# Kernel optimization log

Hardware: AMD Instinct MI355X
Metric: run time of the kernel (lower is better)

The kernel has to match this reference:

```python
import jax, jax.numpy as jnp
import numpy as np

N_NODES = 50000
N_EDGES = 800000
EPS = 1e-5
NEG_SLOPE = 0.2


def _gatv2(x, src, dst, Wl, bl, Wr, br, att, bias, concat, N):
    # PyG GATv2Conv: xl = lin_l(x) (source side), xr = lin_r(x) (target side)
    H, C = att.shape
    xl = (x @ Wl + bl).reshape(N, H, C)
    xr = (x @ Wr + br).reshape(N, H, C)
    # per-edge message: leaky_relu(xl[j] + xr[i]), attention logit = <att, .>
    z = xl[src] + xr[dst]                      # [E, H, C]
    z = jnp.where(z > 0, z, NEG_SLOPE * z)
    logits = jnp.einsum('ehc,hc->eh', z, att)  # [E, H]
    # segment softmax over incoming edges of each target node
    m = jax.lax.stop_gradient(jax.ops.segment_max(logits, dst, num_segments=N))
    p = jnp.exp(logits - m[dst])
    s = jax.ops.segment_sum(p, dst, num_segments=N)
    alpha = p / s[dst]                         # [E, H]
    out = jax.ops.segment_sum(xl[src] * alpha[..., None], dst, num_segments=N)  # [N, H, C]
    out = out.reshape(N, H * C) if concat else out.mean(axis=1)
    return out + bias


def _bn(x, g, b):
    mu = x.mean(axis=0)
    v = x.var(axis=0)
    return (x - mu) * jax.lax.rsqrt(v + EPS) * g + b


def setup_inputs() -> dict:
    key = jax.random.key(0)
    ks = jax.random.split(key, 16)
    x = jax.random.normal(ks[0], (N_NODES, 2), jnp.float32)
    edge_index = jax.random.randint(ks[1], (2, N_EDGES), 0, N_NODES, dtype=jnp.int64)

    def lin(k, i, o):
        return jax.random.normal(k, (i, o), jnp.float32) * (1.0 / np.sqrt(i))

    inp = {'x': x, 'edge_index': edge_index}
    # layer 1: in=2, heads=8, out=16, concat
    inp['W1l'] = lin(ks[2], 2, 128); inp['b1l'] = jnp.zeros((128,), jnp.float32)
    inp['W1r'] = lin(ks[3], 2, 128); inp['b1r'] = jnp.zeros((128,), jnp.float32)
    inp['a1'] = jax.random.normal(ks[4], (8, 16), jnp.float32) * 0.1
    inp['bias1'] = jnp.zeros((128,), jnp.float32)
    inp['g1'] = jnp.ones((128,), jnp.float32); inp['be1'] = jnp.zeros((128,), jnp.float32)
    # layer 2: in=128, heads=4, out=16, concat
    inp['W2l'] = lin(ks[5], 128, 64); inp['b2l'] = jnp.zeros((64,), jnp.float32)
    inp['W2r'] = lin(ks[6], 128, 64); inp['b2r'] = jnp.zeros((64,), jnp.float32)
    inp['a2'] = jax.random.normal(ks[7], (4, 16), jnp.float32) * 0.1
    inp['bias2'] = jnp.zeros((64,), jnp.float32)
    inp['g2'] = jnp.ones((64,), jnp.float32); inp['be2'] = jnp.zeros((64,), jnp.float32)
    # layer 3: in=64, heads=1, out=2, mean (concat=False)
    inp['W3l'] = lin(ks[8], 64, 2); inp['b3l'] = jnp.zeros((2,), jnp.float32)
    inp['W3r'] = lin(ks[9], 64, 2); inp['b3r'] = jnp.zeros((2,), jnp.float32)
    inp['a3'] = jax.random.normal(ks[10], (1, 2), jnp.float32) * 0.1
    inp['bias3'] = jnp.zeros((2,), jnp.float32)
    return inp


def reference(x, edge_index, W1l, b1l, W1r, b1r, a1, bias1, g1, be1,
              W2l, b2l, W2r, b2r, a2, bias2, g2, be2,
              W3l, b3l, W3r, b3r, a3, bias3):
    N = x.shape[0]
    loops = jnp.arange(N, dtype=edge_index.dtype)
    src = jnp.concatenate([edge_index[0], loops])  # add self loops (PyG default)
    dst = jnp.concatenate([edge_index[1], loops])
    h = _gatv2(x, src, dst, W1l, b1l, W1r, b1r, a1, bias1, True, N)
    h = jax.nn.elu(_bn(h, g1, be1))  # dropout is identity in eval
    h = _gatv2(h, src, dst, W2l, b2l, W2r, b2r, a2, bias2, True, N)
    h = jax.nn.elu(_bn(h, g2, be2))
    return _gatv2(h, src, dst, W3l, b3l, W3r, b3r, a3, bias3, False, N)
```

## Files before the change

kernel.cpp:

```cpp
#include <hip/hip_runtime.h>
#include <hip/hip_bf16.h>

#define N_NODES 50000
#define N_E0    800000
#define N_ET    850000
#define EPSBN   1e-5f
#define LOG2E   1.4426950408889634f

#define LEAKY(z) fmaxf((z), 0.2f * (z))

#define OFF_C 0
#define OFF_A (128*N_NODES)
#define OFF_B (192*N_NODES)
#define OFF_STATS (256*N_NODES)
#define OFF_S1R (OFF_STATS + 512)
#define OFF_S2R (OFF_S1R + 16384)
#define OFF_P (OFF_S2R + 8192)
#define N_PARAM_TOT 118312
#define OFF_ROWPTR (OFF_P + N_PARAM_TOT)
#define OFF_DEG    (OFF_ROWPTR + 50001)
#define OFF_CURSOR (OFF_DEG + 50000)
#define OFF_BSUM   (OFF_CURSOR + 50000)
#define OFF_COL    (OFF_BSUM + 256)
#define OFF_FLAGS  (OFF_COL + 850064)
#define OFF_SCNT   (OFF_FLAGS + 2)

#define BK_CAP 131072
#define BK_CHUNK 2048

typedef float v2f __attribute__((ext_vector_type(2)));

__device__ __forceinline__ v2f ld2(const float* p) { return *(const v2f*)p; }
__device__ __forceinline__ v2f fma2(v2f a, v2f b, v2f c) {
    return __builtin_elementwise_fma(a, b, c);
}
__device__ __forceinline__ v2f max2(v2f a, v2f b) {
    return __builtin_elementwise_max(a, b);
}

__device__ __forceinline__ float bf2f(unsigned short u) {
    return __uint_as_float(((unsigned int)u) << 16);
}
__device__ __forceinline__ unsigned short f2bf(float f) {
    unsigned int u = __float_as_uint(f);
    u += 0x7FFFu + ((u >> 16) & 1u);
    return (unsigned short)(u >> 16);
}

__global__ void prep_kernel(const unsigned short* xr, const int* ei, int* flags,
                            int* deg, float* stats, float* s1r, float* s2r, int* scnt,
                            int* col) {
    int i = blockIdx.x * 256 + threadIdx.x;
    if (i < N_NODES) deg[i] = 0;
    if (i < 512) stats[i] = 0.f;
    if (i < 16384) s1r[i] = 0.f;
    if (i < 8192)  s2r[i] = 0.f;
    if (i < 8) scnt[i] = 0;
    if (i < 64) col[N_ET + i] = 0;
    if (blockIdx.x == 0) {
        __shared__ int c1, c2;
        if (threadIdx.x == 0) { c1 = 0; c2 = 0; }
        __syncthreads();
        int t = threadIdx.x;
        int l1 = 0, l2 = 0;
        for (int k = t; k < 2048; k += 256) {
            float v = bf2f(xr[k]);
            if (!(fabsf(v) <= 100.0f)) l1++;
            if (ei[2 * k + 1] != 0) l2++;
        }
        atomicAdd(&c1, l1);
        atomicAdd(&c2, l2);
        __syncthreads();
        if (t == 0) {
            flags[0] = (c1 > 16) ? 1 : 0;
            flags[1] = (c2 == 0) ? 1 : 0;
        }
    }
}

struct ParamPtrs { const void* p[23]; };

__global__ void convert_kernel(ParamPtrs ps, float* dst, const int* flags) {
    const int sizes[23] = {100000, 256,128,256,128,128,128,128,128,
                           8192,64,8192,64,64,64,64,64,
                           128,2,128,2,2,2};
    int g = blockIdx.x * 256 + threadIdx.x;
    if (g >= N_PARAM_TOT) return;
    int t = 0, off = g;
    while (off >= sizes[t]) { off -= sizes[t]; t++; }
    float v;
    if (flags[0]) v = ((const float*)ps.p[t])[off];
    else          v = bf2f(((const unsigned short*)ps.p[t])[off]);
    if (t == 5 || t == 13 || t == 21) v *= LOG2E;
    dst[g] = v;
}

__global__ void bucket_kernel(const int* ei, const int* flags, int* scnt,
                              int* dstb, int* srcb, int* deg) {
    __shared__ int lcnt[8];
    __shared__ int lbase[8];
    int tid = threadIdx.x;
    if (tid < 8) lcnt[tid] = 0;
    __syncthreads();
    int base_e = blockIdx.x * BK_CHUNK;
    int i64 = flags[1];
    int src[8], dst[8], pos[8];
    #pragma unroll
    for (int u = 0; u < 8; u++) {
        int e = base_e + u * 256 + tid;
        if (e < N_ET) {
            int s, d;
            if (e < N_E0) {
                d = i64 ? ei[2 * (N_E0 + e)] : ei[N_E0 + e];
                s = i64 ? ei[2 * e] : ei[e];
            } else { s = d = e - N_E0; }
            src[u] = s; dst[u] = d;
            pos[u] = atomicAdd(&lcnt[d / 6250], 1);
            atomicAdd(&deg[d], 1);
        } else dst[u] = -1;
    }
    __syncthreads();
    if (tid < 8) lbase[tid] = atomicAdd(&scnt[tid], lcnt[tid]);
    __syncthreads();
    #pragma unroll
    for (int u = 0; u < 8; u++) {
        if (dst[u] >= 0) {
            int st = dst[u] / 6250;
            int gp = st * BK_CAP + lbase[st] + pos[u];
            dstb[gp] = dst[u];
            srcb[gp] = src[u];
        }
    }
}

__global__ void scan1_kernel(const int* deg, int* row_ptr, int* bsum) {
    __shared__ int sh[256];
    int i = blockIdx.x * 256 + threadIdx.x;
    int v = (i < N_NODES) ? deg[i] : 0;
    sh[threadIdx.x] = v;
    __syncthreads();
    for (int off = 1; off < 256; off <<= 1) {
        int t = (threadIdx.x >= off) ? sh[threadIdx.x - off] : 0;
        __syncthreads();
        sh[threadIdx.x] += t;
        __syncthreads();
    }
    if (i < N_NODES) row_ptr[i] = sh[threadIdx.x] - v;
    if (threadIdx.x == 255) bsum[blockIdx.x] = sh[255];
}

__global__ void scan23_kernel(int* row_ptr, int* cursor, const int* bsum) {
    __shared__ int sh[256];
    int t = threadIdx.x;
    int v = (t < 196) ? bsum[t] : 0;
    sh[t] = v;
    __syncthreads();
    for (int off = 1; off < 256; off <<= 1) {
        int u = (t >= off) ? sh[t - off] : 0;
        __syncthreads();
        sh[t] += u;
        __syncthreads();
    }
    int prefix = (blockIdx.x == 0) ? 0 : sh[blockIdx.x - 1];
    int i = blockIdx.x * 256 + t;
    if (i < N_NODES) {
        int r = row_ptr[i] + prefix;
        row_ptr[i] = r;
        cursor[i] = r;
    }
    if (i == 0) row_ptr[N_NODES] = N_ET;
}

__global__ void scatter2_kernel(const int* scnt, const int* dstb, const int* srcb,
                                int* cursor, int* col) {
    int stripe = blockIdx.x & 7;
    int bi = blockIdx.x >> 3;
    int cnt = scnt[stripe];
    int off = stripe * BK_CAP;
    for (int t = bi * 256 + threadIdx.x; t < cnt; t += 32 * 256) {
        int d = dstb[off + t];
        int pos = atomicAdd(&cursor[d], 1);
        col[pos] = srcb[off + t];
    }
}

__global__ void __launch_bounds__(256) gather1_kernel(
    const int* row_ptr, const int* col, const float* x,
    const float* W1l, const float* b1l, const float* W1r, const float* b1r,
    const float* att, const float* bias, unsigned int* Cb, float* s1r)
{
    int wv = threadIdx.x >> 6;
    int lane = threadIdx.x & 63;
    int n0 = blockIdx.x * 16 + wv * 4;
    int eslot = lane >> 4;
    int slot  = lane & 15;
    int c0 = slot << 3;

    int rpl = row_ptr[n0 + (lane < 5 ? lane : 4)];
    int r0 = __builtin_amdgcn_readlane(rpl, 0);
    int r1 = __builtin_amdgcn_readlane(rpl, 1);
    int r2 = __builtin_amdgcn_readlane(rpl, 2);
    int r3 = __builtin_amdgcn_readlane(rpl, 3);
    int r4 = __builtin_amdgcn_readlane(rpl, 4);
    int d0 = r1 - r0, d1 = r2 - r1, d2 = r3 - r2, d3 = r4 - r3;

    int ms0 = col[r0 + lane];
    int ms1 = col[r1 + lane];
    int ms2 = col[r2 + lane];
    int ms3 = col[r3 + lane];
    v2f xs0 = ld2(x + 2 * ms0);
    v2f xs1 = ld2(x + 2 * ms1);
    v2f xs2 = ld2(x + 2 * ms2);
    v2f xs3 = ld2(x + 2 * ms3);

    v2f w0[4], w1[4], at[4];
    #pragma unroll
    for (int k = 0; k < 4; k++) {
        w0[k] = ld2(W1l + c0 + 2 * k);
        w1[k] = ld2(W1l + 128 + c0 + 2 * k);
        at[k] = ld2(att + c0 + 2 * k);
    }
    v2f w0o = ld2(W1l + 2 * lane);
    v2f w1o = ld2(W1l + 128 + 2 * lane);
    v2f bo  = ld2(b1l + 2 * lane) + ld2(bias + 2 * lane);

    float bnS0 = 0.f, bnS1 = 0.f, bnQ0 = 0.f, bnQ1 = 0.f;

    auto run_node = [&](int ni, int basei, int degi, v2f xsv) {
        v2f xd = ld2(x + 2 * ni);
        v2f xdx = {xd.x, xd.x}, xdy = {xd.y, xd.y};
        v2f K[4];
        #pragma unroll
        for (int k = 0; k < 4; k++) {
            v2f wr0 = ld2(W1r + c0 + 2 * k);
            v2f wr1 = ld2(W1r + 128 + c0 + 2 * k);
            v2f bb  = ld2(b1r + c0 + 2 * k) + ld2(b1l + c0 + 2 * k);
            K[k] = fma2(xdx, wr0, fma2(xdy, wr1, bb));
        }
        float S0 = 0.f, S1 = 0.f, SP = 0.f;
        int cnt = degi < 64 ? degi : 64;
        for (int jb = 0; jb < cnt; jb += 4) {
            int e = jb + eslot;
            float x0s = __shfl(xsv.x, e, 64);
            float x1s = __shfl(xsv.y, e, 64);
            v2f x0 = {x0s, x0s}, x1 = {x1s, x1s};
            v2f lg = {0.f, 0.f};
            #pragma unroll
            for (int k = 0; k < 4; k++) {
                v2f t = fma2(x1, w1[k], fma2(x0, w0[k], K[k]));
                lg = fma2(max2(t, 0.2f * t), at[k], lg);
            }
            float logit = lg.x + lg.y;
            logit += __shfl_xor(logit, 1, 64);
            float p = (e < cnt) ? exp2f(logit) : 0.f;
            S0 = fmaf(p, x0s, S0);
            S1 = fmaf(p, x1s, S1);
            SP += p;
        }
        for (int j0 = 64; j0 < degi; j0 += 64) {
            int c2 = degi - j0; if (c2 > 64) c2 = 64;
            int m = col[basei + j0 + lane];
            v2f xv = ld2(x + 2 * m);
            for (int jb = 0; jb < c2; jb += 4) {
                int e = jb + eslot;
                float x0s = __shfl(xv.x, e, 64);
                float x1s = __shfl(xv.y, e, 64);
                v2f x0 = {x0s, x0s}, x1 = {x1s, x1s};
                v2f lg = {0.f, 0.f};
                #pragma unroll
                for (int k = 0; k < 4; k++) {
                    v2f t = fma2(x1, w1[k], fma2(x0, w0[k], K[k]));
                    lg = fma2(max2(t, 0.2f * t), at[k], lg);
                }
                float logit = lg.x + lg.y;
                logit += __shfl_xor(logit, 1, 64);
                float p = (e < c2) ? exp2f(logit) : 0.f;
                S0 = fmaf(p, x0s, S0);
                S1 = fmaf(p, x1s, S1);
                SP += p;
            }
        }
        #pragma unroll
        for (int m = 16; m <= 32; m <<= 1) {
            S0 += __shfl_xor(S0, m, 64);
            S1 += __shfl_xor(S1, m, 64);
            SP += __shfl_xor(SP, m, 64);
        }
        float inv = 1.f / SP;
        float t0 = S0 * inv, t1 = S1 * inv;
        int hsrc = (lane >> 3) << 1;
        float t0o = __shfl(t0, hsrc, 64);
        float t1o = __shfl(t1, hsrc, 64);
        float ox = fmaf(w0o.x, t0o, fmaf(w1o.x, t1o, bo.x));
        float oy = fmaf(w0o.y, t0o, fmaf(w1o.y, t1o, bo.y));
        Cb[ni * 64 + lane] = ((unsigned int)f2bf(oy) << 16) | f2bf(ox);
        bnS0 += ox; bnS1 += oy;
        bnQ0 += ox * ox; bnQ1 += oy * oy;
    };

    run_node(n0,     r0, d0, xs0);
    run_node(n0 + 1, r1, d1, xs1);
    run_node(n0 + 2, r2, d2, xs2);
    run_node(n0 + 3, r3, d3, xs3);

    __shared__ float sred[4][128];
    __shared__ float qred[4][128];
    sred[wv][2 * lane]     = bnS0;
    sred[wv][2 * lane + 1] = bnS1;
    qred[wv][2 * lane]     = bnQ0;
    qred[wv][2 * lane + 1] = bnQ1;
    __syncthreads();
    int t = threadIdx.x;
    float a;
    if (t < 128) a = sred[0][t] + sred[1][t] + sred[2][t] + sred[3][t];
    else { int c = t - 128; a = qred[0][c] + qred[1][c] + qred[2][c] + qred[3][c]; }
    atomicAdd(&s1r[(blockIdx.x & 63) * 256 + t], a);
}

__global__ void red1_kernel(const float* s1r, const float* g1, const float* be1,
                            float* stats) {
    __shared__ float ls[256];
    int t = threadIdx.x;
    float a = 0.f;
    for (int r = 0; r < 64; r++) a += s1r[r * 256 + t];
    ls[t] = a;
    __syncthreads();
    if (t < 128) {
        float mu = ls[t] * (1.0f / N_NODES);
        float var = ls[128 + t] * (1.0f / N_NODES) - mu * mu;
        float sc = g1[t] * rsqrtf(var + EPSBN);
        stats[t] = sc;
        stats[128 + t] = be1[t] - mu * sc;
    }
}

__global__ void __launch_bounds__(256) lin2_kernel(
    const unsigned int* Cb, const float* stats, const float* Wl, const float* bl,
    const float* Wr, const float* br, unsigned short* xl2b, float* xr2)
{
    __shared__ float h[64 * 132];
    int tid = threadIdx.x;
    int nb = blockIdx.x * 64;
    for (int i = tid; i < 64 * 64; i += 256) {
        int ni = i >> 6, kp = i & 63;
        int n = nb + ni;
        int k = 2 * kp;
        float v0 = 0.f, v1 = 0.f;
        if (n < N_NODES) {
            unsigned int pk = Cb[n * 64 + kp];
            float b0 = fmaf(__uint_as_float(pk << 16),        stats[k],     stats[128 + k]);
            float b1 = fmaf(__uint_as_float(pk & 0xffff0000u), stats[k + 1], stats[128 + k + 1]);
            v0 = b0 > 0.f ? b0 : __expf(b0) - 1.f;
            v1 = b1 > 0.f ? b1 : __expf(b1) - 1.f;
        }
        h[ni * 132 + k]     = v0;
        h[ni * 132 + k + 1] = v1;
    }
    __syncthreads();
    int kt = (tid & 15) * 4;
    int nt = (tid >> 4) * 4;
    float accl[4][4], accr[4][4];
    #pragma unroll
    for (int i = 0; i < 4; i++) {
        #pragma unroll
        for (int k = 0; k < 4; k++) { accl[i][k] = 0.f; accr[i][k] = 0.f; }
    }
    for (int j = 0; j < 128; j += 4) {
        float4 hv[4];
        #pragma unroll
        for (int i = 0; i < 4; i++)
            hv[i] = *(const float4*)&h[(nt + i) * 132 + j];
        #pragma unroll
        for (int jj = 0; jj < 4; jj++) {
            float4 wl4 = *(const float4*)&Wl[(j + jj) * 64 + kt];
            float4 wr4 = *(const float4*)&Wr[(j + jj) * 64 + kt];
            #pragma unroll
            for (int i = 0; i < 4; i++) {
                float hvv = (jj == 0) ? hv[i].x : (jj == 1) ? hv[i].y :
                            (jj == 2) ? hv[i].z : hv[i].w;
                accl[i][0] += hvv * wl4.x; accl[i][1] += hvv * wl4.y;
                accl[i][2] += hvv * wl4.z; accl[i][3] += hvv * wl4.w;
                accr[i][0] += hvv * wr4.x; accr[i][1] += hvv * wr4.y;
                accr[i][2] += hvv * wr4.z; accr[i][3] += hvv * wr4.w;
            }
        }
    }
    float4 blv = *(const float4*)&bl[kt];
    float4 brv = *(const float4*)&br[kt];
    #pragma unroll
    for (int i = 0; i < 4; i++) {
        int n = nb + nt + i;
        if (n < N_NODES) {
            ushort4 ob;
            ob.x = f2bf(accl[i][0] + blv.x);
            ob.y = f2bf(accl[i][1] + blv.y);
            ob.z = f2bf(accl[i][2] + blv.z);
            ob.w = f2bf(accl[i][3] + blv.w);
            *(ushort4*)&xl2b[n * 64 + kt] = ob;
            float4 o;
            o.x = accr[i][0] + brv.x; o.y = accr[i][1] + brv.y;
            o.z = accr[i][2] + brv.z; o.w = accr[i][3] + brv.w;
            *(float4*)&xr2[n * 64 + kt] = o;
        }
    }
}

__global__ void __launch_bounds__(256) gather2_kernel(
    const int* row_ptr, const int* col, const unsigned short* xl2b, const float* xr2,
    const float* att, const float* bias, float* C, float* s2r)
{
    int gid = blockIdx.x * 256 + threadIdx.x;
    int n = gid >> 6;
    int lane = threadIdx.x & 63;
    int grp = lane >> 4;
    int cidx = lane & 15;
    float4 xrv = *(const float4*)(xr2 + n * 64 + 4 * cidx);
    float4 atv = *(const float4*)(att + 4 * cidx);
    int base = __builtin_amdgcn_readfirstlane(row_ptr[n]);
    int deg  = __builtin_amdgcn_readfirstlane(row_ptr[n + 1]) - base;
    float4 acc = make_float4(0.f, 0.f, 0.f, 0.f);
    float den = 0.f;
    for (int j0 = 0; j0 < deg; j0 += 64) {
        int cnt = deg - j0; if (cnt > 64) cnt = 64;
        int msrc = col[base + j0 + lane];
        for (int j4 = 0; j4 < cnt; j4 += 8) {
            int e0 = j4 + grp, e1 = j4 + 4 + grp;
            int s0 = __shfl(msrc, e0, 64);
            int s1 = __shfl(msrc, e1, 64);
            bool v0 = e0 < cnt, v1 = e1 < cnt;
            s0 = v0 ? s0 : 0;
            s1 = v1 ? s1 : 0;
            uint2 ba = *(const uint2*)(xl2b + (size_t)s0 * 64 + 4 * cidx);
            uint2 bb = *(const uint2*)(xl2b + (size_t)s1 * 64 + 4 * cidx);
            float a0 = __uint_as_float(ba.x << 16);
            float a1 = __uint_as_float(ba.x & 0xffff0000u);
            float a2 = __uint_as_float(ba.y << 16);
            float a3 = __uint_as_float(ba.y & 0xffff0000u);
            float b0 = __uint_as_float(bb.x << 16);
            float b1 = __uint_as_float(bb.x & 0xffff0000u);
            float b2 = __uint_as_float(bb.y << 16);
            float b3 = __uint_as_float(bb.y & 0xffff0000u);
            float pa = LEAKY(a0 + xrv.x) * atv.x;
            pa = fmaf(LEAKY(a1 + xrv.y), atv.y, pa);
            pa = fmaf(LEAKY(a2 + xrv.z), atv.z, pa);
            pa = fmaf(LEAKY(a3 + xrv.w), atv.w, pa);
            float pb = LEAKY(b0 + xrv.x) * atv.x;
            pb = fmaf(LEAKY(b1 + xrv.y), atv.y, pb);
            pb = fmaf(LEAKY(b2 + xrv.z), atv.z, pb);
            pb = fmaf(LEAKY(b3 + xrv.w), atv.w, pb);
            pa += __shfl_xor(pa, 1, 64);
            pa += __shfl_xor(pa, 2, 64);
            pb += __shfl_xor(pb, 1, 64);
            pb += __shfl_xor(pb, 2, 64);
            float ea = v0 ? exp2f(pa) : 0.f;
            float eb = v1 ? exp2f(pb) : 0.f;
            acc.x = fmaf(ea, a0, acc.x); acc.x = fmaf(eb, b0, acc.x);
            acc.y = fmaf(ea, a1, acc.y); acc.y = fmaf(eb, b1, acc.y);
            acc.z = fmaf(ea, a2, acc.z); acc.z = fmaf(eb, b2, acc.z);
            acc.w = fmaf(ea, a3, acc.w); acc.w = fmaf(eb, b3, acc.w);
            den += ea + eb;
        }
    }
    acc.x += __shfl_xor(acc.x, 16, 64); acc.x += __shfl_xor(acc.x, 32, 64);
    acc.y += __shfl_xor(acc.y, 16, 64); acc.y += __shfl_xor(acc.y, 32, 64);
    acc.z += __shfl_xor(acc.z, 16, 64); acc.z += __shfl_xor(acc.z, 32, 64);
    acc.w += __shfl_xor(acc.w, 16, 64); acc.w += __shfl_xor(acc.w, 32, 64);
    den += __shfl_xor(den, 16, 64);
    den += __shfl_xor(den, 32, 64);
    float inv = 1.f / den;
    float4 bi = *(const float4*)(bias + 4 * cidx);
    float4 o;
    o.x = fmaf(acc.x, inv, bi.x);
    o.y = fmaf(acc.y, inv, bi.y);
    o.z = fmaf(acc.z, inv, bi.z);
    o.w = fmaf(acc.w, inv, bi.w);
    if (lane < 16) *(float4*)(C + n * 64 + 4 * cidx) = o;
    __shared__ float sred[4][64];
    __shared__ float qred[4][64];
    int wv = threadIdx.x >> 6;
    if (lane < 16) {
        int c = 4 * cidx;
        sred[wv][c]     = o.x; qred[wv][c]     = o.x * o.x;
        sred[wv][c + 1] = o.y; qred[wv][c + 1] = o.y * o.y;
        sred[wv][c + 2] = o.z; qred[wv][c + 2] = o.z * o.z;
        sred[wv][c + 3] = o.w; qred[wv][c + 3] = o.w * o.w;
    }
    __syncthreads();
    int t = threadIdx.x;
    if (t < 128) {
        float a;
        if (t < 64) a = sred[0][t] + sred[1][t] + sred[2][t] + sred[3][t];
        else { int c = t - 64; a = qred[0][c] + qred[1][c] + qred[2][c] + qred[3][c]; }
        atomicAdd(&s2r[(blockIdx.x & 63) * 128 + t], a);
    }
}

__global__ void red2_kernel(const float* s2r, const float* g2, const float* be2,
                            float* stats) {
    __shared__ float ls[128];
    int t = threadIdx.x;
    float a = 0.f;
    for (int r = 0; r < 64; r++) a += s2r[r * 128 + t];
    ls[t] = a;
    __syncthreads();
    if (t < 64) {
        float mu = ls[t] * (1.0f / N_NODES);
        float var = ls[64 + t] * (1.0f / N_NODES) - mu * mu;
        float sc = g2[t] * rsqrtf(var + EPSBN);
        stats[t] = sc;
        stats[64 + t] = be2[t] - mu * sc;
    }
}

__global__ void __launch_bounds__(256) lin3_kernel(
    const float* C, const float* stats2,
    const float* Wl, const float* bl, const float* Wr, const float* br,
    float* xl3, float* xr3)
{
    int gid = blockIdx.x * 256 + threadIdx.x;
    int n = gid >> 6;
    int lane = threadIdx.x & 63;
    if (n >= N_NODES) return;
    float v = fmaf(C[n * 64 + lane], stats2[lane], stats2[64 + lane]);
    float h = v > 0.f ? v : __expf(v) - 1.f;
    float2 wlv = *(const float2*)(Wl + 2 * lane);
    float2 wrv = *(const float2*)(Wr + 2 * lane);
    float a0 = h * wlv.x, a1 = h * wlv.y;
    float r0 = h * wrv.x, r1 = h * wrv.y;
    #pragma unroll
    for (int m = 1; m < 64; m <<= 1) {
        a0 += __shfl_xor(a0, m, 64);
        a1 += __shfl_xor(a1, m, 64);
        r0 += __shfl_xor(r0, m, 64);
        r1 += __shfl_xor(r1, m, 64);
    }
    if (lane == 0) {
        xl3[2 * n]     = a0 + bl[0];
        xl3[2 * n + 1] = a1 + bl[1];
        xr3[2 * n]     = r0 + br[0];
        xr3[2 * n + 1] = r1 + br[1];
    }
}

__global__ void __launch_bounds__(256) gather3_kernel(
    const int* row_ptr, const int* col,
    const float* xl3, const float* xr3,
    const float* att, const float* bias,
    void* out, const int* flags) {
    int gid = blockIdx.x * 256 + threadIdx.x;
    int n = gid >> 2;
    int q = threadIdx.x & 3;
    if (n >= N_NODES) return;
    float a0 = att[0], a1 = att[1];
    float xr0 = xr3[2 * n], xr1 = xr3[2 * n + 1];
    float acc0 = 0.f, acc1 = 0.f, den = 0.f;
    int e0 = row_ptr[n], e1 = row_ptr[n + 1];
    for (int e = e0 + q; e < e1; e += 4) {
        int src = col[e];
        float2 xs = *(const float2*)(xl3 + 2 * src);
        float z0 = LEAKY(xs.x + xr0);
        float z1 = LEAKY(xs.y + xr1);
        float p = exp2f(fmaf(z0, a0, z1 * a1));
        acc0 = fmaf(p, xs.x, acc0);
        acc1 = fmaf(p, xs.y, acc1);
        den += p;
    }
    acc0 += __shfl_xor(acc0, 1, 64); acc0 += __shfl_xor(acc0, 2, 64);
    acc1 += __shfl_xor(acc1, 1, 64); acc1 += __shfl_xor(acc1, 2, 64);
    den  += __shfl_xor(den, 1, 64);  den  += __shfl_xor(den, 2, 64);
    if (q == 0) {
        float inv = 1.f / den;
        float v0 = fmaf(acc0, inv, bias[0]);
        float v1 = fmaf(acc1, inv, bias[1]);
        if (flags[0]) {
            ((float*)out)[2 * n] = v0;
            ((float*)out)[2 * n + 1] = v1;
        } else {
            ((__hip_bfloat16*)out)[2 * n] = __float2bfloat16(v0);
            ((__hip_bfloat16*)out)[2 * n + 1] = __float2bfloat16(v1);
        }
    }
}

extern "C" void kernel_launch(void* const* d_in, const int* in_sizes, int n_in,
                              void* d_out, int out_size, void* d_ws, size_t ws_size,
                              hipStream_t stream) {
    float* W = (float*)d_ws;
    float* C = W + OFF_C;
    float* A = W + OFF_A;
    float* B = W + OFF_B;
    float* STATS = W + OFF_STATS;
    float* S1R = W + OFF_S1R;
    float* S2R = W + OFF_S2R;
    float* P = W + OFF_P;
    int* ROWPTR = (int*)(W + OFF_ROWPTR);
    int* DEG    = (int*)(W + OFF_DEG);
    int* CURSOR = (int*)(W + OFF_CURSOR);
    int* BSUM   = (int*)(W + OFF_BSUM);
    int* COL    = (int*)(W + OFF_COL);
    int* FLAGS  = (int*)(W + OFF_FLAGS);
    int* SCNT   = (int*)(W + OFF_SCNT);
    int* DSTB   = (int*)(W + OFF_C);
    int* SRCB   = DSTB + 8 * BK_CAP;

    const int* ei = (const int*)d_in[1];

    float* Px  = P;
    float* W1l = Px + 100000; float* b1l = W1l + 256; float* W1r = b1l + 128; float* b1r = W1r + 256;
    float* a1  = b1r + 128;   float* bias1 = a1 + 128; float* g1 = bias1 + 128; float* be1 = g1 + 128;
    float* W2l = be1 + 128;   float* b2l = W2l + 8192; float* W2r = b2l + 64;  float* b2r = W2r + 8192;
    float* a2  = b2r + 64;    float* bias2 = a2 + 64;  float* g2 = bias2 + 64; float* be2 = g2 + 64;
    float* W3l = be2 + 64;    float* b3l = W3l + 128;  float* W3r = b3l + 2;   float* b3r = W3r + 128;
    float* a3  = b3r + 2;     float* bias3 = a3 + 2;

    prep_kernel<<<196, 256, 0, stream>>>((const unsigned short*)d_in[0], ei, FLAGS, DEG, STATS, S1R, S2R, SCNT, COL);

    ParamPtrs ps;
    ps.p[0] = d_in[0];
    for (int j = 1; j < 23; j++) ps.p[j] = d_in[j + 1];
    convert_kernel<<<(N_PARAM_TOT + 255) / 256, 256, 0, stream>>>(ps, P, FLAGS);

    bucket_kernel<<<(N_ET + BK_CHUNK - 1) / BK_CHUNK, 256, 0, stream>>>(ei, FLAGS, SCNT, DSTB, SRCB, DEG);
    scan1_kernel<<<196, 256, 0, stream>>>(DEG, ROWPTR, BSUM);
    scan23_kernel<<<196, 256, 0, stream>>>(ROWPTR, CURSOR, BSUM);
    scatter2_kernel<<<256, 256, 0, stream>>>(SCNT, DSTB, SRCB, CURSOR, COL);

    gather1_kernel<<<N_NODES / 16, 256, 0, stream>>>(ROWPTR, COL, Px, W1l, b1l, W1r, b1r, a1, bias1, (unsigned int*)C, S1R);
    red1_kernel<<<1, 256, 0, stream>>>(S1R, g1, be1, STATS);

    lin2_kernel<<<(N_NODES + 63) / 64, 256, 0, stream>>>((const unsigned int*)C, STATS, W2l, b2l, W2r, b2r, (unsigned short*)A, B);
    gather2_kernel<<<N_NODES * 64 / 256, 256, 0, stream>>>(ROWPTR, COL, (const unsigned short*)A, B, a2, bias2, C, S2R);
    red2_kernel<<<1, 128, 0, stream>>>(S2R, g2, be2, STATS + 256);

    lin3_kernel<<<N_NODES * 64 / 256, 256, 0, stream>>>(C, STATS + 256, W3l, b3l, W3r, b3r, A, B);
    gather3_kernel<<<(N_NODES * 4 + 255) / 256, 256, 0, stream>>>(ROWPTR, COL, A, B, a3, bias3, d_out, FLAGS);
}
```

Before: 324.1 us.

## Compute layer-2 linear projection with split-bf16 MFMA instead of scalar FMAs

Replaces the FP32 scalar-FMA 128x128 projection in lin2_kernel with bf16 MFMA 16x16x32 instructions. Both the activations and the weights are split into high and low bf16 parts, and three MFMAs per tile recover near-FP32 accuracy. A new small wf_kernel prepacks W2l/W2r into the MFMA operand layout. The cost is one extra launch, more LDS for the two split activation buffers, and scalar 2-byte output stores in place of the old vectorized ones.

Result: faster. 312.1 us, median of 2 (-3.7%).

```diff
diff --git a/kernel.cpp b/kernel.cpp
--- a/kernel.cpp
+++ b/kernel.cpp
@@ -24,11 +24,14 @@
 #define OFF_COL    (OFF_BSUM + 256)
 #define OFF_FLAGS  (OFF_COL + 850064)
 #define OFF_SCNT   (OFF_FLAGS + 2)
+#define OFF_WF     (OFF_SCNT + 9)
 
 #define BK_CAP 131072
 #define BK_CHUNK 2048
 
 typedef float v2f __attribute__((ext_vector_type(2)));
+typedef __bf16 bf16x8 __attribute__((ext_vector_type(8)));
+typedef float f32x4 __attribute__((ext_vector_type(4)));
 
 __device__ __forceinline__ v2f ld2(const float* p) { return *(const v2f*)p; }
 __device__ __forceinline__ v2f fma2(v2f a, v2f b, v2f c) {
@@ -93,6 +96,24 @@
     else          v = bf2f(((const unsigned short*)ps.p[t])[off]);
     if (t == 5 || t == 13 || t == 21) v *= LOG2E;
     dst[g] = v;
+}
+
+__global__ void wf_kernel(const float* W2l, const float* W2r,
+                          unsigned short* wfh, unsigned short* wfl) {
+    int g = blockIdx.x * 256 + threadIdx.x;
+    if (g >= 2048) return;
+    int ts = g >> 6;
+    int l  = g & 63;
+    int t = ts >> 2, s = ts & 3;
+    int k0 = 32 * s + 8 * (l >> 4);
+    int c  = 16 * t + (l & 15);
+    #pragma unroll
+    for (int i = 0; i < 8; i++) {
+        float v = (c < 64) ? W2l[(k0 + i) * 64 + c] : W2r[(k0 + i) * 64 + (c - 64)];
+        unsigned short hi = f2bf(v);
+        wfh[g * 8 + i] = hi;
+        wfl[g * 8 + i] = f2bf(v - bf2f(hi));
+    }
 }
 
 __global__ void bucket_kernel(const int* ei, const int* flags, int* scnt,
@@ -335,10 +356,13 @@
 }
 
 __global__ void __launch_bounds__(256) lin2_kernel(
-    const unsigned int* Cb, const float* stats, const float* Wl, const float* bl,
-    const float* Wr, const float* br, unsigned short* xl2b, float* xr2)
+    const unsigned int* Cb, const float* stats,
+    const unsigned short* wfh, const unsigned short* wfl,
+    const float* bl, const float* br,
+    unsigned short* xl2b, float* xr2)
 {
-    __shared__ float h[64 * 132];
+    __shared__ __align__(16) unsigned int hA[64 * 68];
+    __shared__ __align__(16) unsigned int hL[64 * 68];
     int tid = threadIdx.x;
     int nb = blockIdx.x * 64;
     for (int i = tid; i < 64 * 64; i += 256) {
@@ -353,54 +377,46 @@
             v0 = b0 > 0.f ? b0 : __expf(b0) - 1.f;
             v1 = b1 > 0.f ? b1 : __expf(b1) - 1.f;
         }
-        h[ni * 132 + k]     = v0;
-        h[ni * 132 + k + 1] = v1;
-    }
-    __syncthreads();
-    int kt = (tid & 15) * 4;
-    int nt = (tid >> 4) * 4;
-    float accl[4][4], accr[4][4];
-    #pragma unroll
-    for (int i = 0; i < 4; i++) {
+        unsigned short h0 = f2bf(v0), h1 = f2bf(v1);
+        unsigned short l0 = f2bf(v0 - bf2f(h0));
+        unsigned short l1 = f2bf(v1 - bf2f(h1));
+        hA[ni * 68 + kp] = (unsigned int)h0 | ((unsigned int)h1 << 16);
+        hL[ni * 68 + kp] = (unsigned int)l0 | ((unsigned int)l1 << 16);
+    }
+    __syncthreads();
+    int wv = tid >> 6;
+    int lane = tid & 63;
+    int g = lane >> 4, lrow = lane & 15;
+    f32x4 acc[8];
+    #pragma unroll
+    for (int t = 0; t < 8; t++) acc[t] = (f32x4){0.f, 0.f, 0.f, 0.f};
+    #pragma unroll
+    for (int s = 0; s < 4; s++) {
+        int aoff = (wv * 16 + lrow) * 272 + s * 64 + g * 16;
+        bf16x8 ah = *(const bf16x8*)((const char*)hA + aoff);
+        bf16x8 al = *(const bf16x8*)((const char*)hL + aoff);
         #pragma unroll
-        for (int k = 0; k < 4; k++) { accl[i][k] = 0.f; accr[i][k] = 0.f; }
-    }
-    for (int j = 0; j < 128; j += 4) {
-        float4 hv[4];
+        for (int t = 0; t < 8; t++) {
+            int bi = ((t * 4 + s) * 64 + lane) * 8;
+            bf16x8 bh = *(const bf16x8*)(wfh + bi);
+            bf16x8 bo = *(const bf16x8*)(wfl + bi);
+            acc[t] = __builtin_amdgcn_mfma_f32_16x16x32_bf16(ah, bh, acc[t], 0, 0, 0);
+            acc[t] = __builtin_amdgcn_mfma_f32_16x16x32_bf16(ah, bo, acc[t], 0, 0, 0);
+            acc[t] = __builtin_amdgcn_mfma_f32_16x16x32_bf16(al, bh, acc[t], 0, 0, 0);
+        }
+    }
+    #pragma unroll
+    for (int t = 0; t < 8; t++) {
+        int ch = 16 * t + lrow;
+        float bias = (t < 4) ? bl[ch] : br[ch - 64];
         #pragma unroll
-        for (int i = 0; i < 4; i++)
-            hv[i] = *(const float4*)&h[(nt + i) * 132 + j];
-        #pragma unroll
-        for (int jj = 0; jj < 4; jj++) {
-            float4 wl4 = *(const float4*)&Wl[(j + jj) * 64 + kt];
-            float4 wr4 = *(const float4*)&Wr[(j + jj) * 64 + kt];
-            #pragma unroll
-            for (int i = 0; i < 4; i++) {
-                float hvv = (jj == 0) ? hv[i].x : (jj == 1) ? hv[i].y :
-                            (jj == 2) ? hv[i].z : hv[i].w;
-                accl[i][0] += hvv * wl4.x; accl[i][1] += hvv * wl4.y;
-                accl[i][2] += hvv * wl4.z; accl[i][3] += hvv * wl4.w;
-                accr[i][0] += hvv * wr4.x; accr[i][1] += hvv * wr4.y;
-                accr[i][2] += hvv * wr4.z; accr[i][3] += hvv * wr4.w;
+        for (int r = 0; r < 4; r++) {
+            int node = nb + wv * 16 + g * 4 + r;
+            if (node < N_NODES) {
+                float v = acc[t][r] + bias;
+                if (t < 4) xl2b[node * 64 + ch] = f2bf(v);
+                else       xr2[node * 64 + ch - 64] = v;
             }
-        }
-    }
-    float4 blv = *(const float4*)&bl[kt];
-    float4 brv = *(const float4*)&br[kt];
-    #pragma unroll
-    for (int i = 0; i < 4; i++) {
-        int n = nb + nt + i;
-        if (n < N_NODES) {
-            ushort4 ob;
-            ob.x = f2bf(accl[i][0] + blv.x);
-            ob.y = f2bf(accl[i][1] + blv.y);
-            ob.z = f2bf(accl[i][2] + blv.z);
-            ob.w = f2bf(accl[i][3] + blv.w);
-            *(ushort4*)&xl2b[n * 64 + kt] = ob;
-            float4 o;
-            o.x = accr[i][0] + brv.x; o.y = accr[i][1] + brv.y;
-            o.z = accr[i][2] + brv.z; o.w = accr[i][3] + brv.w;
-            *(float4*)&xr2[n * 64 + kt] = o;
         }
     }
 }
@@ -602,6 +618,8 @@
     int* SCNT   = (int*)(W + OFF_SCNT);
     int* DSTB   = (int*)(W + OFF_C);
     int* SRCB   = DSTB + 8 * BK_CAP;
+    unsigned short* WFH = (unsigned short*)(W + OFF_WF);
+    unsigned short* WFL = WFH + 16384;
 
     const int* ei = (const int*)d_in[1];
 
@@ -619,6 +637,7 @@
     ps.p[0] = d_in[0];
     for (int j = 1; j < 23; j++) ps.p[j] = d_in[j + 1];
     convert_kernel<<<(N_PARAM_TOT + 255) / 256, 256, 0, stream>>>(ps, P, FLAGS);
+    wf_kernel<<<8, 256, 0, stream>>>(W2l, W2r, WFH, WFL);
 
     bucket_kernel<<<(N_ET + BK_CHUNK - 1) / BK_CHUNK, 256, 0, stream>>>(ei, FLAGS, SCNT, DSTB, SRCB, DEG);
     scan1_kernel<<<196, 256, 0, stream>>>(DEG, ROWPTR, BSUM);
@@ -628,7 +647,7 @@
     gather1_kernel<<<N_NODES / 16, 256, 0, stream>>>(ROWPTR, COL, Px, W1l, b1l, W1r, b1r, a1, bias1, (unsigned int*)C, S1R);
     red1_kernel<<<1, 256, 0, stream>>>(S1R, g1, be1, STATS);
 
-    lin2_kernel<<<(N_NODES + 63) / 64, 256, 0, stream>>>((const unsigned int*)C, STATS, W2l, b2l, W2r, b2r, (unsigned short*)A, B);
+    lin2_kernel<<<(N_NODES + 63) / 64, 256, 0, stream>>>((const unsigned int*)C, STATS, WFH, WFL, b2l, b2r, (unsigned short*)A, B);
     gather2_kernel<<<N_NODES * 64 / 256, 256, 0, stream>>>(ROWPTR, COL, (const unsigned short*)A, B, a2, bias2, C, S2R);
     red2_kernel<<<1, 128, 0, stream>>>(S2R, g2, be2, STATS + 256);
 
```
